# Kernel tuning notes

Hardware: AMD Instinct MI355X
Metric: run time of the kernel (lower is better)

The kernel has to match this reference:

```python
import jax, jax.numpy as jnp
import numpy as np

H = 1024   # hidden_size
I = 4096   # intermediate_size
E = 8      # num_local_experts
K = 2      # num_experts_per_tok
B, S = 2, 2048


def setup_inputs() -> dict:
    key = jax.random.key(0)
    ks = jax.random.split(key, 7)
    init = lambda k, shape, fan_in: (jax.random.normal(k, shape, jnp.float32)
                                     / np.float32(np.sqrt(fan_in)))
    return {
        "x": jax.random.normal(ks[0], (B, S, H), jnp.float32),
        "router_gate": init(ks[1], (E, H), H),   # router for gate_proj
        "w_gate": init(ks[2], (E, I, H), H),     # expert weights gate_proj
        "router_up": init(ks[3], (E, H), H),     # router for up_proj
        "w_up": init(ks[4], (E, I, H), H),       # expert weights up_proj
        "router_down": init(ks[5], (E, I), I),   # router for down_proj
        "w_down": init(ks[6], (E, H, I), I),     # expert weights down_proj
    }


def _moe_linear(x, router_w, expert_w):
    """Top-K routed linear. x:[T,din] router_w:[E,din] expert_w:[E,dout,din]."""
    n_exp = router_w.shape[0]
    logits = x @ router_w.T                      # [T, E]
    vals, idx = jax.lax.top_k(logits, K)         # [T, K]
    probs = jax.nn.softmax(vals, axis=-1)        # softmax over selected experts
    onehot = jax.nn.one_hot(idx, n_exp, dtype=x.dtype)    # [T, K, E]
    combine = jnp.einsum('tk,tke->te', probs, onehot)     # [T, E] sparse combine weights
    out = jnp.zeros((x.shape[0], expert_w.shape[1]), x.dtype)
    for e in range(n_exp):  # fixed small expert count
        out = out + combine[:, e:e + 1] * (x @ expert_w[e].T)
    return out


def reference(x, router_gate, w_gate, router_up, w_up, router_down, w_down):
    b, s, h = x.shape
    xt = x.reshape(b * s, h)                     # tokens [T, H]
    g = _moe_linear(xt, router_gate, w_gate)     # [T, I]
    u = _moe_linear(xt, router_up, w_up)         # [T, I]
    inter = jax.nn.silu(g) * u                   # SwiGLU
    d = _moe_linear(inter, router_down, w_down)  # [T, H]
    return d.reshape(b, s, h)
```

## Files before the change

### kernel.cpp

```cpp
#include <hip/hip_runtime.h>
#include <cmath>

typedef float    f32x4 __attribute__((ext_vector_type(4)));
typedef _Float16 f16x8 __attribute__((ext_vector_type(8)));
typedef _Float16 f16x4 __attribute__((ext_vector_type(4)));

#define T_NUM 4096
#define H_DIM 1024
#define I_DIM 4096
#define MAXTILES 40

#define M_COUNTS   0
#define M_CURSORS  48
#define M_OFFSETS  96
#define M_NTILES   144
#define M_TILE_E   152
#define M_TILE_M   392
#define M_TOPKI    1024
#define M_TOPKP    25600
#define M_STOK     50176
#define M_SPRB     74752

__device__ __forceinline__ float wave_sum(float v) {
  v += __shfl_xor(v, 32);
  v += __shfl_xor(v, 16);
  v += __shfl_xor(v, 8);
  v += __shfl_xor(v, 4);
  v += __shfl_xor(v, 2);
  v += __shfl_xor(v, 1);
  return v;
}

__device__ __forceinline__ void topk_write(int* meta, int layer, int t, const float* v) {
  int e0 = 0; float v0 = v[0];
  #pragma unroll
  for (int e = 1; e < 8; ++e) { if (v[e] > v0) { v0 = v[e]; e0 = e; } }
  int e1 = 0; float v1 = -3.4e38f;
  #pragma unroll
  for (int e = 0; e < 8; ++e) { if (e != e0 && v[e] > v1) { v1 = v[e]; e1 = e; } }
  float ex = expf(v1 - v0);
  float p0 = 1.f / (1.f + ex);
  float p1 = ex / (1.f + ex);
  meta[M_TOPKI + (layer * T_NUM + t) * 2    ] = e0;
  meta[M_TOPKI + (layer * T_NUM + t) * 2 + 1] = e1;
  ((float*)meta)[M_TOPKP + (layer * T_NUM + t) * 2    ] = p0;
  ((float*)meta)[M_TOPKP + (layer * T_NUM + t) * 2 + 1] = p1;
}

__global__ __launch_bounds__(256) void router_gu(const float* __restrict__ x,
    const float* __restrict__ Rg, const float* __restrict__ Ru, int* __restrict__ meta)
{
  int w = threadIdx.x >> 6, lane = threadIdx.x & 63;
  int t = blockIdx.x * 4 + w;
  const float* xr = x + (size_t)t * H_DIM + lane * 4;
  f32x4 xv[4];
  #pragma unroll
  for (int c = 0; c < 4; ++c) xv[c] = *(const f32x4*)(xr + c * 256);
  float lg[8], lu[8];
  #pragma unroll
  for (int e = 0; e < 8; ++e) {
    const float* rg = Rg + (size_t)e * H_DIM + lane * 4;
    const float* ru = Ru + (size_t)e * H_DIM + lane * 4;
    float sg = 0.f, su = 0.f;
    #pragma unroll
    for (int c = 0; c < 4; ++c) {
      f32x4 a = *(const f32x4*)(rg + c * 256);
      f32x4 b = *(const f32x4*)(ru + c * 256);
      sg += a[0]*xv[c][0] + a[1]*xv[c][1] + a[2]*xv[c][2] + a[3]*xv[c][3];
      su += b[0]*xv[c][0] + b[1]*xv[c][1] + b[2]*xv[c][2] + b[3]*xv[c][3];
    }
    lg[e] = wave_sum(sg);
    lu[e] = wave_sum(su);
  }
  if (lane == 0) {
    topk_write(meta, 0, t, lg);
    topk_write(meta, 1, t, lu);
  }
}

__global__ __launch_bounds__(256) void route_finalize(int* __restrict__ meta, int l0, int nl) {
  __shared__ int cnt_s[32];
  __shared__ int off_s[32];
  __shared__ int cur_s[32];
  int tid = threadIdx.x;
  if (tid < 32) { cnt_s[tid] = 0; cur_s[tid] = 0; }
  __syncthreads();
  for (int t = tid; t < T_NUM; t += 256) {
    for (int l = l0; l < l0 + nl; ++l) {
      int li = l - l0;
      #pragma unroll
      for (int k = 0; k < 2; ++k) {
        int e = meta[M_TOPKI + (l * T_NUM + t) * 2 + k];
        atomicAdd(&cnt_s[li * 16 + k * 8 + e], 1);
      }
    }
  }
  __syncthreads();
  if (tid == 0) {
    for (int l = l0; l < l0 + nl; ++l) {
      int li = l - l0;
      int off = 0;
      for (int k = 0; k < 2; ++k) {
        int nt = 0;
        for (int e = 0; e < 8; ++e) {
          int s = (l * 2 + k) * 8 + e;
          int c = cnt_s[li * 16 + k * 8 + e];
          meta[M_COUNTS + s] = c;
          meta[M_OFFSETS + s] = off;
          off_s[li * 16 + k * 8 + e] = off;
          for (int m = 0; m < c; m += 128) {
            meta[M_TILE_E + (l * 2 + k) * MAXTILES + nt] = e;
            meta[M_TILE_M + (l * 2 + k) * MAXTILES + nt] = m;
            ++nt;
          }
          off += c;
        }
        meta[M_NTILES + l * 2 + k] = nt;
      }
    }
  }
  __syncthreads();
  for (int t = tid; t < T_NUM; t += 256) {
    for (int l = l0; l < l0 + nl; ++l) {
      int li = l - l0;
      #pragma unroll
      for (int k = 0; k < 2; ++k) {
        int e = meta[M_TOPKI + (l * T_NUM + t) * 2 + k];
        float p = ((float*)meta)[M_TOPKP + (l * T_NUM + t) * 2 + k];
        int si = li * 16 + k * 8 + e;
        int pos = off_s[si] + atomicAdd(&cur_s[si], 1);
        meta[M_STOK + l * 8192 + pos] = t;
        ((float*)meta)[M_SPRB + l * 8192 + pos] = p;
      }
    }
  }
}

template<int SPLITS>
__global__ __launch_bounds__(256) void convert_w(const float* __restrict__ W,
    _Float16* __restrict__ Whi, _Float16* __restrict__ Wlo, int NB, int KT)
{
  size_t g = (size_t)blockIdx.x * 256 + threadIdx.x;
  int c   = (int)(g >> 9);
  int rem = (int)(g & 511);
  int fq = rem >> 7, r = rem & 127;
  int e  = c / (NB * KT);
  int nb = (c / KT) % NB;
  int kt = c - (c / KT) * KT;
  int K = KT * 32, N = NB * 128;
  const float* src = W + ((size_t)(e * N + nb * 128 + r)) * K + kt * 32 + fq * 8;
  f32x4 v0 = *(const f32x4*)src;
  f32x4 v1 = *(const f32x4*)(src + 4);
  f16x8 h, l;
  #pragma unroll
  for (int q = 0; q < 8; ++q) {
    float v = (q < 4) ? v0[q] : v1[q - 4];
    _Float16 hv = (_Float16)v;
    h[q] = hv;
    l[q] = (_Float16)(v - (float)hv);
  }
  size_t dst = (size_t)c * 4096 + (size_t)rem * 8;
  *(f16x8*)(Whi + dst) = h;
  if constexpr (SPLITS == 3) *(f16x8*)(Wlo + dst) = l;
}

__global__ __launch_bounds__(256) void gather_a(const float* __restrict__ X,
    _Float16* __restrict__ Apass, const int* __restrict__ meta, int layer, int kk)
{
  int pass = layer * 2 + kk;
  int tile = blockIdx.x >> 5;
  int kt   = blockIdx.x & 31;
  if (tile >= meta[M_NTILES + pass]) return;
  int e    = meta[M_TILE_E + pass * MAXTILES + tile];
  int m0   = meta[M_TILE_M + pass * MAXTILES + tile];
  int sidx = pass * 8 + e;
  int cnt  = meta[M_COUNTS + sidx];
  int seg  = meta[M_OFFSETS + sidx];
  const int* stok = meta + M_STOK + layer * 8192 + seg;
  size_t cb = ((size_t)tile * 32 + kt) * 8192;
  #pragma unroll
  for (int j = 0; j < 2; ++j) {
    int idx = threadIdx.x * 2 + j;
    int fq = idx >> 7, row = idx & 127;
    int m = m0 + row; if (m >= cnt) m = cnt - 1;
    const float* src = X + (size_t)stok[m] * H_DIM + kt * 32 + fq * 8;
    f32x4 v0 = *(const f32x4*)src;
    f32x4 v1 = *(const f32x4*)(src + 4);
    f16x8 h, l;
    #pragma unroll
    for (int q = 0; q < 8; ++q) {
      float v = (q < 4) ? v0[q] : v1[q - 4];
      _Float16 hv = (_Float16)v;
      h[q] = hv;
      l[q] = (_Float16)(v - (float)hv);
    }
    *(f16x8*)(Apass + cb + (size_t)idx * 8) = h;
    *(f16x8*)(Apass + cb + 4096 + (size_t)idx * 8) = l;
  }
}

__global__ __launch_bounds__(256) void gather_d(const _Float16* __restrict__ Gi,
    _Float16* __restrict__ Ad, const int* __restrict__ meta, int kk)
{
  int pass = 4 + kk;
  int tile = blockIdx.x >> 7;
  int kt   = blockIdx.x & 127;
  if (tile >= meta[M_NTILES + pass]) return;
  int e    = meta[M_TILE_E + pass * MAXTILES + tile];
  int m0   = meta[M_TILE_M + pass * MAXTILES + tile];
  int sidx = pass * 8 + e;
  int cnt  = meta[M_COUNTS + sidx];
  int seg  = meta[M_OFFSETS + sidx];
  const int* stok = meta + M_STOK + 2 * 8192 + seg;
  size_t cb = ((size_t)tile * 128 + kt) * 4096;
  #pragma unroll
  for (int j = 0; j < 2; ++j) {
    int idx = threadIdx.x * 2 + j;
    int fq = idx >> 7, row = idx & 127;
    int m = m0 + row; if (m >= cnt) m = cnt - 1;
    f16x8 h = *(const f16x8*)(Gi + (size_t)stok[m] * I_DIM + kt * 32 + fq * 8);
    *(f16x8*)(Ad + cb + (size_t)idx * 8) = h;
  }
}

__device__ __forceinline__ void gload16(const _Float16* g, _Float16* l) {
  __builtin_amdgcn_global_load_lds(
      (const __attribute__((address_space(1))) void*)g,
      (__attribute__((address_space(3))) void*)l, 16, 0, 0);
}

template<int SPLITS, int ADD, int N, int NB, int STEPS, int SPLITK>
__global__ __launch_bounds__(256, 3) void moe_gemm9(
    const _Float16* __restrict__ Aimg,
    const _Float16* __restrict__ Whi, const _Float16* __restrict__ Wlo,
    float* __restrict__ Out, float* __restrict__ Scr,
    const int* __restrict__ meta, int layer, int kk)
{
  constexpr int NWG = MAXTILES * NB * SPLITK;
  constexpr int Q8  = NWG / 8;
  constexpr int WCH = (SPLITS == 3) ? 1 : 2;

  int xcd  = (int)blockIdx.x & 7;
  int slot = (int)blockIdx.x >> 3;
  int nper = (int)gridDim.x >> 3;
  int pass = layer * 2 + kk;
  int ntiles = meta[M_NTILES + pass];

  __shared__ __align__(16) _Float16 sA[3 * 8192];

  int tid = threadIdx.x, lane = tid & 63, w = tid >> 6;
  int wr = w >> 1, wc = w & 1, fr = lane & 15, fq = lane >> 4;
  int aoff = (fq * 128 + wr * 64 + fr) * 8;

  for (int base = slot; base < Q8; base += nper) {
    int logical = xcd * Q8 + base;
    int kc = 0, rem = logical;
    if constexpr (SPLITK == 2) { kc = logical / (MAXTILES * NB); rem = logical - kc * (MAXTILES * NB); }
    int tx = rem / NB;
    int ny = rem - tx * NB;
    if (tx >= ntiles) continue;

    int e    = meta[M_TILE_E + pass * MAXTILES + tx];
    int m0   = meta[M_TILE_M + pass * MAXTILES + tx];
    int sidx = pass * 8 + e;
    int cnt  = meta[M_COUNTS + sidx];
    int seg  = meta[M_OFFSETS + sidx];
    int n0   = ny * 128;

    const int*   stok = meta + M_STOK + layer * 8192 + seg;
    const float* sprb = (const float*)meta + M_SPRB + layer * 8192 + seg;

    const _Float16* At = Aimg + ((size_t)tx * SPLITK + kc) * STEPS * 8192;
    size_t wpanel = (size_t)(e * NB + ny) * (STEPS * WCH * SPLITK) * 4096;
    int kb = kc * STEPS * WCH;
    const _Float16* WhL = Whi + wpanel + (size_t)kb * 4096 + (fq * 128 + wc * 64 + fr) * 8;
    const _Float16* WlL = Wlo + wpanel + (size_t)kb * 4096 + (fq * 128 + wc * 64 + fr) * 8;

    auto stageA = [&](int it, int slot2) {
      const _Float16* s0 = At + (size_t)it * 8192 + w * 1024 + lane * 8;
      _Float16* d0 = sA + slot2 * 8192 + w * 1024;
      gload16(s0,        d0);
      gload16(s0 + 512,  d0 + 512);
      gload16(s0 + 4096, d0 + 4096);
      gload16(s0 + 4608, d0 + 4608);
    };
    auto loadW = [&](int it, f16x8 (&wh)[WCH][4], f16x8 (&wl)[1][4]) {
      #pragma unroll
      for (int c = 0; c < WCH; ++c) {
        size_t cb = (size_t)(it * WCH + c) * 4096;
        #pragma unroll
        for (int ni = 0; ni < 4; ++ni) wh[c][ni] = *(const f16x8*)(WhL + cb + ni * 128);
      }
      if constexpr (SPLITS == 3) {
        size_t cb = (size_t)it * 4096;
        #pragma unroll
        for (int ni = 0; ni < 4; ++ni) wl[0][ni] = *(const f16x8*)(WlL + cb + ni * 128);
      }
    };

    f32x4 acc[4][4];
    #pragma unroll
    for (int i = 0; i < 4; ++i)
      #pragma unroll
      for (int j = 0; j < 4; ++j) acc[i][j] = f32x4{0.f, 0.f, 0.f, 0.f};

    f16x8 w0h[WCH][4], w0l[1][4], w1h[WCH][4], w1l[1][4];
    int rc = 0, rs = 2;

    auto step = [&](int it, f16x8 (&cwh)[WCH][4], f16x8 (&cwl)[1][4],
                    f16x8 (&nwh)[WCH][4], f16x8 (&nwl)[1][4]) {
      int it2 = (it + 2 < STEPS) ? it + 2 : STEPS - 1;
      int it1 = (it + 1 < STEPS) ? it + 1 : STEPS - 1;
      stageA(it2, rs);
      loadW(it1, nwh, nwl);
      __builtin_amdgcn_sched_barrier(0);

      const _Float16* A0 = sA + rc * 8192;
      __builtin_amdgcn_s_setprio(1);
      if constexpr (SPLITS == 3) {
        f16x8 ah[4], al[4];
        #pragma unroll
        for (int mi = 0; mi < 4; ++mi) ah[mi] = *(const f16x8*)(A0 + aoff + mi * 128);
        #pragma unroll
        for (int mi = 0; mi < 4; ++mi) al[mi] = *(const f16x8*)(A0 + 4096 + aoff + mi * 128);
        #pragma unroll
        for (int mi = 0; mi < 4; ++mi)
          #pragma unroll
          for (int ni = 0; ni < 4; ++ni)
            acc[mi][ni] = __builtin_amdgcn_mfma_f32_16x16x32_f16(ah[mi], cwh[0][ni], acc[mi][ni], 0, 0, 0);
        #pragma unroll
        for (int mi = 0; mi < 4; ++mi)
          #pragma unroll
          for (int ni = 0; ni < 4; ++ni)
            acc[mi][ni] = __builtin_amdgcn_mfma_f32_16x16x32_f16(ah[mi], cwl[0][ni], acc[mi][ni], 0, 0, 0);
        #pragma unroll
        for (int mi = 0; mi < 4; ++mi)
          #pragma unroll
          for (int ni = 0; ni < 4; ++ni)
            acc[mi][ni] = __builtin_amdgcn_mfma_f32_16x16x32_f16(al[mi], cwh[0][ni], acc[mi][ni], 0, 0, 0);
      } else {
        #pragma unroll
        for (int c = 0; c < WCH; ++c) {
          f16x8 ah[4];
          #pragma unroll
          for (int mi = 0; mi < 4; ++mi) ah[mi] = *(const f16x8*)(A0 + c * 4096 + aoff + mi * 128);
          #pragma unroll
          for (int mi = 0; mi < 4; ++mi)
            #pragma unroll
            for (int ni = 0; ni < 4; ++ni)
              acc[mi][ni] = __builtin_amdgcn_mfma_f32_16x16x32_f16(ah[mi], cwh[c][ni], acc[mi][ni], 0, 0, 0);
        }
      }
      __builtin_amdgcn_s_setprio(0);

      __builtin_amdgcn_sched_barrier(0);
      asm volatile("s_waitcnt vmcnt(12)" ::: "memory");
      __builtin_amdgcn_s_barrier();
      __builtin_amdgcn_sched_barrier(0);
      rc = (rc == 2) ? 0 : rc + 1;
      rs = (rs == 2) ? 0 : rs + 1;
    };

    asm volatile("s_waitcnt vmcnt(0)" ::: "memory");
    __builtin_amdgcn_s_barrier();
    stageA(0, 0);
    stageA(1 < STEPS ? 1 : 0, 1);
    loadW(0, w0h, w0l);
    __builtin_amdgcn_sched_barrier(0);
    asm volatile("s_waitcnt vmcnt(12)" ::: "memory");
    __builtin_amdgcn_s_barrier();
    __builtin_amdgcn_sched_barrier(0);

    for (int it = 0; it < STEPS; it += 2) {
      step(it,     w0h, w0l, w1h, w1l);
      step(it + 1, w1h, w1l, w0h, w0l);
    }

    float* dst = (SPLITK == 2 && kc == 1) ? Scr : Out;
    #pragma unroll
    for (int mi = 0; mi < 4; ++mi) {
      #pragma unroll
      for (int jj = 0; jj < 4; ++jj) {
        int lm = wr * 64 + mi * 16 + fq * 4 + jj;
        int gm = m0 + lm;
        if (gm < cnt) {
          int tok = stok[gm];
          float p = sprb[gm];
          float* orow = dst + (size_t)tok * N + n0 + wc * 64 + fr;
          #pragma unroll
          for (int ni = 0; ni < 4; ++ni) {
            float v = p * acc[mi][ni][jj];
            if constexpr (ADD) orow[ni * 16] += v; else orow[ni * 16] = v;
          }
        }
      }
    }
  }
}

__global__ __launch_bounds__(256) void swiglu_router(const float* __restrict__ g,
    const float* __restrict__ u, const float* __restrict__ Rd,
    _Float16* __restrict__ gi, int* __restrict__ meta)
{
  int t = blockIdx.x, tid = threadIdx.x;
  float part[8];
  #pragma unroll
  for (int e = 0; e < 8; ++e) part[e] = 0.f;
  const float* gr = g + (size_t)t * I_DIM;
  const float* ur = u + (size_t)t * I_DIM;
  _Float16*    ir = gi + (size_t)t * I_DIM;
  #pragma unroll
  for (int cc = 0; cc < 4; ++cc) {
    int i = cc * 1024 + tid * 4;
    f32x4 gv = *(const f32x4*)(gr + i);
    f32x4 uv = *(const f32x4*)(ur + i);
    f32x4 iv;
    f16x4 hv;
    #pragma unroll
    for (int j = 0; j < 4; ++j) {
      float xx = gv[j];
      iv[j] = (xx / (1.f + expf(-xx))) * uv[j];
      hv[j] = (_Float16)iv[j];
    }
    *(f16x4*)(ir + i) = hv;
    #pragma unroll
    for (int e = 0; e < 8; ++e) {
      f32x4 rv = *(const f32x4*)(Rd + (size_t)e * I_DIM + i);
      part[e] += rv[0]*iv[0] + rv[1]*iv[1] + rv[2]*iv[2] + rv[3]*iv[3];
    }
  }
  __shared__ float red[4][8];
  int w = tid >> 6, lane = tid & 63;
  #pragma unroll
  for (int e = 0; e < 8; ++e) {
    float s = wave_sum(part[e]);
    if (lane == 0) red[w][e] = s;
  }
  __syncthreads();
  if (tid == 0) {
    float lg[8];
    #pragma unroll
    for (int e = 0; e < 8; ++e) lg[e] = red[0][e] + red[1][e] + red[2][e] + red[3][e];
    topk_write(meta, 2, t, lg);
  }
}

__global__ __launch_bounds__(256) void combine_kernel(float* __restrict__ out,
                                                      const float* __restrict__ scr)
{
  int i = blockIdx.x * 1024 + threadIdx.x * 4;
  f32x4 a = *(const f32x4*)(out + i);
  f32x4 b = *(const f32x4*)(scr + i);
  #pragma unroll
  for (int j = 0; j < 4; ++j) a[j] += b[j];
  *(f32x4*)(out + i) = a;
}

extern "C" void kernel_launch(void* const* d_in, const int* in_sizes, int n_in,
                              void* d_out, int out_size, void* d_ws, size_t ws_size,
                              hipStream_t stream)
{
  const float* x  = (const float*)d_in[0];
  const float* Rg = (const float*)d_in[1];
  const float* Wg = (const float*)d_in[2];
  const float* Ru = (const float*)d_in[3];
  const float* Wu = (const float*)d_in[4];
  const float* Rd = (const float*)d_in[5];
  const float* Wd = (const float*)d_in[6];
  float* out = (float*)d_out;
  char* ws = (char*)d_ws;

  _Float16* Wth = (_Float16*)ws;
  _Float16* Wtl = (_Float16*)(ws + (size_t)67108864);
  float* g   = (float*)(ws + (size_t)134217728);
  float* u   = (float*)(ws + (size_t)201326592);
  int*  meta = (int*)(ws + (size_t)268435456);
  _Float16* Apass = (_Float16*)(ws + (size_t)269484032);
  _Float16* gi    = (_Float16*)Wtl;
  _Float16* Ad    = (_Float16*)(ws + (size_t)201326592);
  float* dscr     = (float*)(ws + (size_t)269484032);

  router_gu<<<dim3(T_NUM / 4), 256, 0, stream>>>(x, Rg, Ru, meta);
  route_finalize<<<dim3(1), 256, 0, stream>>>(meta, 0, 2);

  convert_w<3><<<dim3(16384), 256, 0, stream>>>(Wg, Wth, Wtl, 32, 32);
  gather_a<<<dim3(MAXTILES * 32), 256, 0, stream>>>(x, Apass, meta, 0, 0);
  moe_gemm9<3, 0, I_DIM, 32, 32, 1><<<dim3(768), 256, 0, stream>>>(
      Apass, Wth, Wtl, g, g, meta, 0, 0);
  gather_a<<<dim3(MAXTILES * 32), 256, 0, stream>>>(x, Apass, meta, 0, 1);
  moe_gemm9<3, 1, I_DIM, 32, 32, 1><<<dim3(768), 256, 0, stream>>>(
      Apass, Wth, Wtl, g, g, meta, 0, 1);

  convert_w<3><<<dim3(16384), 256, 0, stream>>>(Wu, Wth, Wtl, 32, 32);
  gather_a<<<dim3(MAXTILES * 32), 256, 0, stream>>>(x, Apass, meta, 1, 0);
  moe_gemm9<3, 0, I_DIM, 32, 32, 1><<<dim3(768), 256, 0, stream>>>(
      Apass, Wth, Wtl, u, u, meta, 1, 0);
  gather_a<<<dim3(MAXTILES * 32), 256, 0, stream>>>(x, Apass, meta, 1, 1);
  moe_gemm9<3, 1, I_DIM, 32, 32, 1><<<dim3(768), 256, 0, stream>>>(
      Apass, Wth, Wtl, u, u, meta, 1, 1);

  swiglu_router<<<dim3(T_NUM), 256, 0, stream>>>(g, u, Rd, gi, meta);
  route_finalize<<<dim3(1), 256, 0, stream>>>(meta, 2, 1);

  convert_w<1><<<dim3(16384), 256, 0, stream>>>(Wd, Wth, Wth, 8, 128);
  gather_d<<<dim3(MAXTILES * 128), 256, 0, stream>>>(gi, Ad, meta, 0);
  moe_gemm9<1, 0, H_DIM, 8, 32, 2><<<dim3(768), 256, 0, stream>>>(
      Ad, Wth, Wth, out, dscr, meta, 2, 0);
  gather_d<<<dim3(MAXTILES * 128), 256, 0, stream>>>(gi, Ad, meta, 1);
  moe_gemm9<1, 1, H_DIM, 8, 32, 2><<<dim3(768), 256, 0, stream>>>(
      Ad, Wth, Wth, out, dscr, meta, 2, 1);
  combine_kernel<<<dim3(T_NUM), 256, 0, stream>>>(out, dscr);
}
```

Before: 1.052 ms.

## Fuse weight conversion with gathers and overlap next-pass gather inside GEMM launches

Weight conversion and activation gather now run in one launch, and each GEMM launch gets extra blocks that gather the A operand for the following pass into a second buffer. This cuts kernel launches and lets gather traffic overlap GEMM compute. To do this the workspace is reassigned so the g/u regions serve as double buffers for the gathered operands, which adds aliasing risk between passes. The up-projection path gathers inside the conversion launch in a different order than the gate path.

```diff
diff --git a/kernel.cpp b/kernel.cpp
--- a/kernel.cpp
+++ b/kernel.cpp
@@ -9,6 +9,7 @@
 #define H_DIM 1024
 #define I_DIM 4096
 #define MAXTILES 40
+#define GEMMBLK 768
 
 #define M_COUNTS   0
 #define M_CURSORS  48
@@ -137,10 +138,10 @@
 }
 
 template<int SPLITS>
-__global__ __launch_bounds__(256) void convert_w(const float* __restrict__ W,
-    _Float16* __restrict__ Whi, _Float16* __restrict__ Wlo, int NB, int KT)
-{
-  size_t g = (size_t)blockIdx.x * 256 + threadIdx.x;
+__device__ __forceinline__ void convert_w_body(const float* __restrict__ W,
+    _Float16* __restrict__ Whi, _Float16* __restrict__ Wlo, int NB, int KT, int blk)
+{
+  size_t g = (size_t)blk * 256 + threadIdx.x;
   int c   = (int)(g >> 9);
   int rem = (int)(g & 511);
   int fq = rem >> 7, r = rem & 127;
@@ -164,15 +165,15 @@
   if constexpr (SPLITS == 3) *(f16x8*)(Wlo + dst) = l;
 }
 
-__global__ __launch_bounds__(256) void gather_a(const float* __restrict__ X,
-    _Float16* __restrict__ Apass, const int* __restrict__ meta, int layer, int kk)
+__device__ __forceinline__ void gather_a_body(const float* __restrict__ X,
+    _Float16* __restrict__ Apass, const int* __restrict__ meta, int layer, int kk, int gb)
 {
   int pass = layer * 2 + kk;
-  int tile = blockIdx.x >> 5;
-  int kt   = blockIdx.x & 31;
+  int tile = gb >> 5;
+  int kt   = gb & 31;
   if (tile >= meta[M_NTILES + pass]) return;
+  int m0   = meta[M_TILE_M + pass * MAXTILES + tile];
   int e    = meta[M_TILE_E + pass * MAXTILES + tile];
-  int m0   = meta[M_TILE_M + pass * MAXTILES + tile];
   int sidx = pass * 8 + e;
   int cnt  = meta[M_COUNTS + sidx];
   int seg  = meta[M_OFFSETS + sidx];
@@ -199,15 +200,15 @@
   }
 }
 
-__global__ __launch_bounds__(256) void gather_d(const _Float16* __restrict__ Gi,
-    _Float16* __restrict__ Ad, const int* __restrict__ meta, int kk)
+__device__ __forceinline__ void gather_d_body(const _Float16* __restrict__ Gi,
+    _Float16* __restrict__ Ad, const int* __restrict__ meta, int kk, int gb)
 {
   int pass = 4 + kk;
-  int tile = blockIdx.x >> 7;
-  int kt   = blockIdx.x & 127;
+  int tile = gb >> 7;
+  int kt   = gb & 127;
   if (tile >= meta[M_NTILES + pass]) return;
+  int m0   = meta[M_TILE_M + pass * MAXTILES + tile];
   int e    = meta[M_TILE_E + pass * MAXTILES + tile];
-  int m0   = meta[M_TILE_M + pass * MAXTILES + tile];
   int sidx = pass * 8 + e;
   int cnt  = meta[M_COUNTS + sidx];
   int seg  = meta[M_OFFSETS + sidx];
@@ -223,36 +224,65 @@
   }
 }
 
+__global__ __launch_bounds__(256) void fused_cw3_ga(const float* __restrict__ W,
+    _Float16* __restrict__ Whi, _Float16* __restrict__ Wlo,
+    const float* __restrict__ X, _Float16* __restrict__ Atgt,
+    const int* __restrict__ meta, int layer, int kk)
+{
+  int b = (int)blockIdx.x;
+  if (b < 16384) convert_w_body<3>(W, Whi, Wlo, 32, 32, b);
+  else gather_a_body(X, Atgt, meta, layer, kk, b - 16384);
+}
+
+__global__ __launch_bounds__(256) void fused_cw1_gd(const float* __restrict__ W,
+    _Float16* __restrict__ Whi,
+    const _Float16* __restrict__ Gi, _Float16* __restrict__ Adt,
+    const int* __restrict__ meta, int kk)
+{
+  int b = (int)blockIdx.x;
+  if (b < 16384) convert_w_body<1>(W, Whi, Whi, 8, 128, b);
+  else gather_d_body(Gi, Adt, meta, kk, b - 16384);
+}
+
 __device__ __forceinline__ void gload16(const _Float16* g, _Float16* l) {
   __builtin_amdgcn_global_load_lds(
       (const __attribute__((address_space(1))) void*)g,
       (__attribute__((address_space(3))) void*)l, 16, 0, 0);
 }
 
-template<int SPLITS, int ADD, int N, int NB, int STEPS, int SPLITK>
-__global__ __launch_bounds__(256, 3) void moe_gemm9(
+template<int SPLITS, int ADD, int N, int NB, int STEPS, int SPLITK, int AUX>
+__global__ __launch_bounds__(256, 3) void moe_gemm_aux(
     const _Float16* __restrict__ Aimg,
     const _Float16* __restrict__ Whi, const _Float16* __restrict__ Wlo,
     float* __restrict__ Out, float* __restrict__ Scr,
-    const int* __restrict__ meta, int layer, int kk)
+    const int* __restrict__ meta, int layer, int kk,
+    const void* __restrict__ aux_src, _Float16* __restrict__ aux_dst,
+    int alayer, int akk)
 {
   constexpr int NWG = MAXTILES * NB * SPLITK;
   constexpr int Q8  = NWG / 8;
   constexpr int WCH = (SPLITS == 3) ? 1 : 2;
+  constexpr int NPER = GEMMBLK / 8;
+
+  __shared__ __align__(16) _Float16 sA[3 * 8192];
+
+  if ((int)blockIdx.x >= GEMMBLK) {
+    int gb = (int)blockIdx.x - GEMMBLK;
+    if constexpr (AUX == 0) gather_a_body((const float*)aux_src, aux_dst, meta, alayer, akk, gb);
+    else                    gather_d_body((const _Float16*)aux_src, aux_dst, meta, akk, gb);
+    return;
+  }
 
   int xcd  = (int)blockIdx.x & 7;
   int slot = (int)blockIdx.x >> 3;
-  int nper = (int)gridDim.x >> 3;
   int pass = layer * 2 + kk;
   int ntiles = meta[M_NTILES + pass];
-
-  __shared__ __align__(16) _Float16 sA[3 * 8192];
 
   int tid = threadIdx.x, lane = tid & 63, w = tid >> 6;
   int wr = w >> 1, wc = w & 1, fr = lane & 15, fq = lane >> 4;
   int aoff = (fq * 128 + wr * 64 + fr) * 8;
 
-  for (int base = slot; base < Q8; base += nper) {
+  for (int base = slot; base < Q8; base += NPER) {
     int logical = xcd * Q8 + base;
     int kc = 0, rem = logical;
     if constexpr (SPLITK == 2) { kc = logical / (MAXTILES * NB); rem = logical - kc * (MAXTILES * NB); }
@@ -475,39 +505,35 @@
   float* g   = (float*)(ws + (size_t)134217728);
   float* u   = (float*)(ws + (size_t)201326592);
   int*  meta = (int*)(ws + (size_t)268435456);
-  _Float16* Apass = (_Float16*)(ws + (size_t)269484032);
-  _Float16* gi    = (_Float16*)Wtl;
-  _Float16* Ad    = (_Float16*)(ws + (size_t)201326592);
-  float* dscr     = (float*)(ws + (size_t)269484032);
+  _Float16* A0 = (_Float16*)(ws + (size_t)269484032);
+  _Float16* A1 = (_Float16*)u;
+  _Float16* gi = (_Float16*)Wtl;
+  _Float16* Ad0 = (_Float16*)u;
+  _Float16* Ad1 = (_Float16*)g;
+  float* dscr = (float*)A0;
 
   router_gu<<<dim3(T_NUM / 4), 256, 0, stream>>>(x, Rg, Ru, meta);
   route_finalize<<<dim3(1), 256, 0, stream>>>(meta, 0, 2);
 
-  convert_w<3><<<dim3(16384), 256, 0, stream>>>(Wg, Wth, Wtl, 32, 32);
-  gather_a<<<dim3(MAXTILES * 32), 256, 0, stream>>>(x, Apass, meta, 0, 0);
-  moe_gemm9<3, 0, I_DIM, 32, 32, 1><<<dim3(768), 256, 0, stream>>>(
-      Apass, Wth, Wtl, g, g, meta, 0, 0);
-  gather_a<<<dim3(MAXTILES * 32), 256, 0, stream>>>(x, Apass, meta, 0, 1);
-  moe_gemm9<3, 1, I_DIM, 32, 32, 1><<<dim3(768), 256, 0, stream>>>(
-      Apass, Wth, Wtl, g, g, meta, 0, 1);
-
-  convert_w<3><<<dim3(16384), 256, 0, stream>>>(Wu, Wth, Wtl, 32, 32);
-  gather_a<<<dim3(MAXTILES * 32), 256, 0, stream>>>(x, Apass, meta, 1, 0);
-  moe_gemm9<3, 0, I_DIM, 32, 32, 1><<<dim3(768), 256, 0, stream>>>(
-      Apass, Wth, Wtl, u, u, meta, 1, 0);
-  gather_a<<<dim3(MAXTILES * 32), 256, 0, stream>>>(x, Apass, meta, 1, 1);
-  moe_gemm9<3, 1, I_DIM, 32, 32, 1><<<dim3(768), 256, 0, stream>>>(
-      Apass, Wth, Wtl, u, u, meta, 1, 1);
+  fused_cw3_ga<<<dim3(16384 + MAXTILES * 32), 256, 0, stream>>>(Wg, Wth, Wtl, x, A0, meta, 0, 0);
+  moe_gemm_aux<3, 0, I_DIM, 32, 32, 1, 0><<<dim3(GEMMBLK + MAXTILES * 32), 256, 0, stream>>>(
+      A0, Wth, Wtl, g, g, meta, 0, 0, x, A1, 0, 1);
+  moe_gemm_aux<3, 1, I_DIM, 32, 32, 1, 0><<<dim3(GEMMBLK + MAXTILES * 32), 256, 0, stream>>>(
+      A1, Wth, Wtl, g, g, meta, 0, 1, x, A0, 1, 0);
+  fused_cw3_ga<<<dim3(16384), 256, 0, stream>>>(Wu, Wth, Wtl, x, A0, meta, 0, 0);
+  moe_gemm_aux<3, 0, I_DIM, 32, 32, 1, 0><<<dim3(GEMMBLK), 256, 0, stream>>>(
+      A0, Wth, Wtl, u, u, meta, 1, 0, x, A0, 0, 0);
+  fused_cw3_ga<<<dim3(16384 + MAXTILES * 32), 256, 0, stream>>>(Wu, Wth, Wtl, x, A0, meta, 1, 1);
+  moe_gemm_aux<3, 1, I_DIM, 32, 32, 1, 0><<<dim3(GEMMBLK), 256, 0, stream>>>(
+      A0, Wth, Wtl, u, u, meta, 1, 1, x, A0, 0, 0);
 
   swiglu_router<<<dim3(T_NUM), 256, 0, stream>>>(g, u, Rd, gi, meta);
   route_finalize<<<dim3(1), 256, 0, stream>>>(meta, 2, 1);
 
-  convert_w<1><<<dim3(16384), 256, 0, stream>>>(Wd, Wth, Wth, 8, 128);
-  gather_d<<<dim3(MAXTILES * 128), 256, 0, stream>>>(gi, Ad, meta, 0);
-  moe_gemm9<1, 0, H_DIM, 8, 32, 2><<<dim3(768), 256, 0, stream>>>(
-      Ad, Wth, Wth, out, dscr, meta, 2, 0);
-  gather_d<<<dim3(MAXTILES * 128), 256, 0, stream>>>(gi, Ad, meta, 1);
-  moe_gemm9<1, 1, H_DIM, 8, 32, 2><<<dim3(768), 256, 0, stream>>>(
-      Ad, Wth, Wth, out, dscr, meta, 2, 1);
+  fused_cw1_gd<<<dim3(16384 + MAXTILES * 128), 256, 0, stream>>>(Wd, Wth, gi, Ad0, meta, 0);
+  moe_gemm_aux<1, 0, H_DIM, 8, 32, 2, 1><<<dim3(GEMMBLK + MAXTILES * 128), 256, 0, stream>>>(
+      Ad0, Wth, Wth, out, dscr, meta, 2, 0, gi, Ad1, 0, 1);
+  moe_gemm_aux<1, 1, H_DIM, 8, 32, 2, 1><<<dim3(GEMMBLK), 256, 0, stream>>>(
+      Ad1, Wth, Wth, out, dscr, meta, 2, 1, gi, Ad1, 0, 1);
   combine_kernel<<<dim3(T_NUM), 256, 0, stream>>>(out, dscr);
 }
```

Result: slower. 1.096 ms (+4.2%).
